# Optimization experiments

Hardware: AMD Instinct MI355X
Metric: run time of the kernel (lower is better)

Reference implementation:

```python
import jax, jax.numpy as jnp
import numpy as np

B, T = 64, 512
V, D, H = 50000, 256, 256  # vocab, word-embed dim, LSTM hidden


def _lstm_dir(x, Wih, Whh, bih, bhh):
    """Unidirectional LSTM over time (PyTorch gate order i,f,g,o). x: [B,T,D_in] -> [B,T,H]."""
    xp = jnp.einsum('btd,gd->btg', x, Wih) + bih + bhh  # precompute input projections [B,T,4H]
    xp = xp.transpose(1, 0, 2)  # [T,B,4H]
    Hh = Whh.shape[1]
    h0 = jnp.zeros((x.shape[0], Hh), x.dtype)

    def step(carry, xt):
        h, c = carry
        g = xt + h @ Whh.T
        i, f, gg, o = jnp.split(g, 4, axis=-1)
        c = jax.nn.sigmoid(f) * c + jax.nn.sigmoid(i) * jnp.tanh(gg)
        h = jax.nn.sigmoid(o) * jnp.tanh(c)
        return (h, c), h

    _, hs = jax.lax.scan(step, (h0, h0), xp)
    return hs.transpose(1, 0, 2)  # [B,T,H]


def _bidir(x, rev_idx, pf, pb):
    """Length-aware bidirectional layer: reverse only the valid prefix (emulates pack_padded_sequence)."""
    hf = _lstm_dir(x, *pf)
    xr = jnp.take_along_axis(x, rev_idx[..., None], axis=1)   # reversed valid prefix
    hb = _lstm_dir(xr, *pb)
    hb = jnp.take_along_axis(hb, rev_idx[..., None], axis=1)  # flip back (involution on valid part)
    return jnp.concatenate([hf, hb], axis=-1)  # [B,T,2H]


def setup_inputs() -> dict:
    key = jax.random.key(0)
    ks = jax.random.split(key, 24)
    x = jax.random.randint(ks[0], (B, T), 0, V - 1)          # avoid padding_idx = V-1
    sentlen = jax.random.randint(ks[1], (B,), 1, T + 1)       # ragged lengths in [1, T]
    embed = (jax.random.normal(ks[2], (V, D), jnp.float32) * 0.1).at[V - 1].set(0.0)
    inp = {"x": x, "sentlen": sentlen, "embed": embed}
    k = 3
    for layer, in_dim in [(0, D), (1, 2 * H)]:
        for d in ["f", "b"]:
            s = 1.0 / np.sqrt(H)
            inp[f"Wih{layer}{d}"] = jax.random.uniform(ks[k], (4 * H, in_dim), jnp.float32, -s, s); k += 1
            inp[f"Whh{layer}{d}"] = jax.random.uniform(ks[k], (4 * H, H), jnp.float32, -s, s); k += 1
            inp[f"bih{layer}{d}"] = jax.random.uniform(ks[k], (4 * H,), jnp.float32, -s, s); k += 1
            inp[f"bhh{layer}{d}"] = jax.random.uniform(ks[k], (4 * H,), jnp.float32, -s, s); k += 1
    return inp


def reference(x, sentlen, embed,
              Wih0f, Whh0f, bih0f, bhh0f, Wih0b, Whh0b, bih0b, bhh0b,
              Wih1f, Whh1f, bih1f, bhh1f, Wih1b, Whh1b, bih1b, bhh1b):
    emb = embed[x]  # [B,T,D]; dropout is a no-op in eval mode
    t = jnp.arange(x.shape[1])
    valid = t[None, :] < sentlen[:, None]                       # [B,T]
    rev_idx = jnp.where(valid, sentlen[:, None] - 1 - t[None, :], t[None, :])
    h1 = _bidir(emb, rev_idx, (Wih0f, Whh0f, bih0f, bhh0f), (Wih0b, Whh0b, bih0b, bhh0b))
    h2 = _bidir(h1, rev_idx, (Wih1f, Whh1f, bih1f, bhh1f), (Wih1b, Whh1b, bih1b, bhh1b))
    # ragged max-pool over valid positions (replaces the per-sample Python loop)
    feat = jnp.max(jnp.where(valid[..., None], h2, -jnp.inf), axis=1)  # [B,2H]
    return feat[None]  # [1,B,2H]
```

## Files before the change

kernel.cpp:

```cpp
#include <hip/hip_runtime.h>
#include <stdint.h>
#include <stddef.h>

#define BATCH 64
#define TT    512
#define DIM   256
#define HID   256
#define MROWS (BATCH*TT)

typedef unsigned short u16;
typedef unsigned int u32;
typedef __attribute__((ext_vector_type(8))) short  short8;
typedef __attribute__((ext_vector_type(4))) float  f32x4;
typedef __attribute__((ext_vector_type(4))) int    int4v;
typedef __attribute__((ext_vector_type(4))) unsigned short u16x4;

__device__ __forceinline__ u16 bf16_hi(float f) {
    union { float f; unsigned u; } v; v.f = f;
    unsigned r = v.u + 0x7fffu + ((v.u >> 16) & 1u);
    return (u16)(r >> 16);
}
__device__ __forceinline__ float bf16f(u16 b) {
    union { unsigned u; float f; } v; v.u = ((unsigned)b) << 16;
    return v.f;
}
__device__ __forceinline__ float fsigmoid(float x) { return 1.f / (1.f + __expf(-x)); }
__device__ __forceinline__ float ftanh(float x) {
    x = fminf(15.f, fmaxf(-15.f, x));
    float e = __expf(2.f * x);
    return (e - 1.f) / (e + 1.f);
}

__global__ __launch_bounds__(256) void k_prep(
    const float* __restrict__ Wih0f, const float* __restrict__ Whh0f, const float* __restrict__ bih0f, const float* __restrict__ bhh0f,
    const float* __restrict__ Wih0b, const float* __restrict__ Whh0b, const float* __restrict__ bih0b, const float* __restrict__ bhh0b,
    const float* __restrict__ Wih1f, const float* __restrict__ Whh1f, const float* __restrict__ bih1f, const float* __restrict__ bhh1f,
    const float* __restrict__ Wih1b, const float* __restrict__ Whh1b, const float* __restrict__ bih1b, const float* __restrict__ bhh1b,
    u16* __restrict__ WihQ0hi, u16* __restrict__ WihQ0lo,
    u16* __restrict__ WhhQ0hi, u16* __restrict__ WhhQ0lo,
    u16* __restrict__ WihQ1hi, u16* __restrict__ WihQ1lo,
    u16* __restrict__ WhhQ1hi, u16* __restrict__ WhhQ1lo,
    float* __restrict__ bsum, u32* __restrict__ hxp)
{
    const int i = blockIdx.x * 256 + threadIdx.x;
    if (i < 2621440) {
        const float* srcf; const float* srcb; u16* dhi; u16* dlo; int off; int K;
        if      (i <  524288) { srcf = Wih0f; srcb = Wih0b; dhi = WihQ0hi; dlo = WihQ0lo; off = i;           K = 256; }
        else if (i < 1048576) { srcf = Whh0f; srcb = Whh0b; dhi = WhhQ0hi; dlo = WhhQ0lo; off = i -  524288; K = 256; }
        else if (i < 2097152) { srcf = Wih1f; srcb = Wih1b; dhi = WihQ1hi; dlo = WihQ1lo; off = i - 1048576; K = 512; }
        else                  { srcf = Whh1f; srcb = Whh1b; dhi = WhhQ1hi; dlo = WhhQ1lo; off = i - 2097152; K = 256; }
        const int SZ = 1024 * K;
        const int dd = off / SZ;
        const int o  = off - dd * SZ;
        const int pr = o / K;
        const int k  = o - pr * K;
        const int s  = pr >> 6;
        const int ww = (pr >> 4) & 3;
        const int m  = pr & 15;
        const int src_row = (m & 3) * 256 + s * 16 + ww * 4 + (m >> 2);
        const float v = (dd ? srcb : srcf)[src_row * K + k];
        const u16 h = bf16_hi(v);
        dhi[off] = h;
        dlo[off] = bf16_hi(v - bf16f(h));
    } else if (i < 2621440 + 4096) {
        const int j = i - 2621440;
        const float* bihs[4] = { bih0f, bih0b, bih1f, bih1b };
        const float* bhhs[4] = { bhh0f, bhh0b, bhh1f, bhh1b };
        const int ld = j >> 10, k = j & 1023;
        bsum[j] = bihs[ld][k] + bhhs[ld][k];
    } else if (i < 2621440 + 4096 + 131072) {
        const int j = i - (2621440 + 4096);
        hxp[j] = ((j >> 15) & 1) ? 0x00010000u : 0u;
    }
}

__global__ __launch_bounds__(256) void k_gather(
    const int* __restrict__ x, const float* __restrict__ embed, u16* __restrict__ A0)
{
    const int row = blockIdx.x * 4 + (threadIdx.x >> 6);
    const int col = (threadIdx.x & 63) * 4;
    const int xi = x[row];
    const f32x4 v = *(const f32x4*)(embed + (size_t)xi * DIM + col);
    u16x4 h;
    #pragma unroll
    for (int i = 0; i < 4; i++) h[i] = bf16_hi(v[i]);
    *(u16x4*)(A0 + (size_t)row * DIM + col) = h;
}

template<int KIN, bool WRITE_H, bool POOL>
__global__ __launch_bounds__(256, 1) void k_lstm(
    const u16* __restrict__ Xin,
    const u16* __restrict__ WhhHi, const u16* __restrict__ WhhLo,
    const u16* __restrict__ WihHi, const u16* __restrict__ WihLo,
    const float* __restrict__ bsum,
    const int* __restrict__ slen,
    u16* __restrict__ H0,
    float* __restrict__ outp,
    u32* __restrict__ hx)
{
    constexpr int KV = KIN / 32;
    constexpr int CR = KIN / 8;
    constexpr int NST = (16 * CR) / 256;

    const int bid = blockIdx.x;
    const int s = bid >> 3;
    const int d = (bid >> 2) & 1;
    const int c = bid & 3;
    const int tid = threadIdx.x;
    const int l = tid & 63, w = tid >> 6;

    __shared__ u16 xs[16 * KIN];
    __shared__ u16 hs_hi[16 * 256];
    __shared__ u16 hs_lo[16 * 256];
    __shared__ u32 ho_pack[16 * 17];
    __shared__ int lens_sh[16];
    __shared__ int maxlen_sh;

    if (tid < 16) lens_sh[tid] = slen[c * 16 + tid];
    __syncthreads();
    if (tid == 0) {
        int m = 0;
        #pragma unroll
        for (int i = 0; i < 16; i++) m = max(m, lens_sh[i]);
        maxlen_sh = m;
    }
    __syncthreads();
    const int maxlen = maxlen_sh;

    const int wblk = (d * 16 + s) * 4 + w;
    short8 wfh[8], wfl[8];
    #pragma unroll
    for (int kv = 0; kv < 8; kv++) {
        const size_t off = (size_t)(wblk * 16 + (l & 15)) * 256 + kv * 32 + ((l >> 4) << 3);
        wfh[kv] = *(const short8*)(WhhHi + off);
        wfl[kv] = *(const short8*)(WhhLo + off);
    }
    short8 uih[KV], uil[KV];
    #pragma unroll
    for (int kv = 0; kv < KV; kv++) {
        const size_t off = (size_t)(wblk * 16 + (l & 15)) * KIN + kv * 32 + ((l >> 4) << 3);
        uih[kv] = *(const short8*)(WihHi + off);
        uil[kv] = *(const short8*)(WihLo + off);
    }
    #pragma unroll
    for (int kv = 0; kv < 8; kv++) asm volatile("" : "+v"(wfh[kv]), "+v"(wfl[kv]));
    #pragma unroll
    for (int kv = 0; kv < KV; kv++) asm volatile("" : "+v"(uih[kv]), "+v"(uil[kv]));

    const int q_u  = l >> 4;
    const int bi_m = l & 15;
    const int unit = s * 16 + w * 4 + q_u;
    float bias_g[4];
    #pragma unroll
    for (int g = 0; g < 4; g++) bias_g[g] = bsum[d * 1024 + g * 256 + unit];

    float creg = 0.f, mx = -1e30f;
    const int swz = bi_m & 7;
    const int klane = l >> 4;
    const int len_m = lens_sh[bi_m];

    for (int t = 0; t < maxlen; ++t) {
        short8 xreg[NST];
        #pragma unroll
        for (int p = 0; p < NST; p++) {
            const int idx = p * 256 + tid;
            const int bi = idx / CR;
            const int ch = idx - bi * CR;
            const int len_b = lens_sh[bi];
            const int pos = (d == 0) ? t : ((t < len_b) ? (len_b - 1 - t) : t);
            xreg[p] = *(const short8*)(Xin + ((size_t)(c * 16 + bi) * TT + pos) * KIN + ch * 8);
            asm volatile("" : "+v"(xreg[p]));
        }

        if (t == 0) {
            const short8 z = {0,0,0,0,0,0,0,0};
            for (int i = tid; i < 512; i += 256) {
                ((short8*)hs_hi)[i] = z;
                ((short8*)hs_lo)[i] = z;
            }
        } else {
            const u32* gbase = hx + (((size_t)(t & 1) * 2 + d) * 64 + c * 16) * 256;
            const u32* p0 = gbase + tid * 4;
            const u32* p1 = p0 + 1024;
            const u32* p2 = p0 + 2048;
            const u32* p3 = p0 + 3072;
            const int expect = (t >> 1) & 1;
            int4v w0, w1, w2, w3;
            int rounds = 0;
            for (;;) {
                asm volatile(
                    "global_load_dwordx4 %0, %4, off sc0 sc1\n\t"
                    "global_load_dwordx4 %1, %5, off sc0 sc1\n\t"
                    "global_load_dwordx4 %2, %6, off sc0 sc1\n\t"
                    "global_load_dwordx4 %3, %7, off sc0 sc1"
                    : "=&v"(w0), "=&v"(w1), "=&v"(w2), "=&v"(w3)
                    : "v"(p0), "v"(p1), "v"(p2), "v"(p3)
                    : "memory");
                asm volatile("s_waitcnt vmcnt(0)"
                    : "+v"(w0), "+v"(w1), "+v"(w2), "+v"(w3) :: "memory");
                u32 aw = 0xFFFFFFFFu, ow = 0u;
                #pragma unroll
                for (int j = 0; j < 4; j++) {
                    aw &= (u32)w0[j]; ow |= (u32)w0[j];
                    aw &= (u32)w1[j]; ow |= (u32)w1[j];
                    aw &= (u32)w2[j]; ow |= (u32)w2[j];
                    aw &= (u32)w3[j]; ow |= (u32)w3[j];
                }
                const int ok = expect ? (int)((aw >> 16) & 1u)
                                      : (int)(((ow >> 16) & 1u) ^ 1u);
                if (__all(ok)) break;
                if (++rounds > (1 << 17)) break;
                __builtin_amdgcn_s_sleep(1);
            }
            const int u0 = (tid & 63) * 4;
            const int ch = u0 >> 3;
            const int co = u0 & 7;
            int4v wq[4] = {w0, w1, w2, w3};
            #pragma unroll
            for (int qq = 0; qq < 4; qq++) {
                const int bi = qq * 4 + (tid >> 6);
                u16x4 hi4, lo4;
                #pragma unroll
                for (int j = 0; j < 4; j++) {
                    const u32 wd = (u32)wq[qq][j];
                    hi4[j] = (u16)(wd & 0xFFFFu);
                    lo4[j] = (u16)(wd >> 16);
                }
                *(u16x4*)(hs_hi + bi * 256 + (ch ^ (bi & 7)) * 8 + co) = hi4;
                *(u16x4*)(hs_lo + bi * 256 + (ch ^ (bi & 7)) * 8 + co) = lo4;
            }
        }
        #pragma unroll
        for (int p = 0; p < NST; p++) {
            const int idx = p * 256 + tid;
            const int bi = idx / CR;
            const int ch = idx - bi * CR;
            *(short8*)(xs + bi * KIN + (ch ^ (bi & 7)) * 8) = xreg[p];
        }
        __syncthreads();

        f32x4 acc_a = {0.f,0.f,0.f,0.f}, acc_b = {0.f,0.f,0.f,0.f}, acc_c = {0.f,0.f,0.f,0.f};
        #pragma unroll
        for (int kv = 0; kv < 8; kv++) {
            const int kc = kv * 4 + klane;
            const short8 bh = *(const short8*)(hs_hi + bi_m * 256 + (kc ^ swz) * 8);
            const short8 bl = *(const short8*)(hs_lo + bi_m * 256 + (kc ^ swz) * 8);
            acc_a = __builtin_amdgcn_mfma_f32_16x16x32_bf16(wfh[kv], bh, acc_a, 0, 0, 0);
            acc_b = __builtin_amdgcn_mfma_f32_16x16x32_bf16(wfl[kv], bh, acc_b, 0, 0, 0);
            acc_c = __builtin_amdgcn_mfma_f32_16x16x32_bf16(wfh[kv], bl, acc_c, 0, 0, 0);
        }
        #pragma unroll
        for (int kv = 0; kv < KV; kv++) {
            const int kc = kv * 4 + klane;
            const short8 bx = *(const short8*)(xs + bi_m * KIN + (kc ^ swz) * 8);
            acc_a = __builtin_amdgcn_mfma_f32_16x16x32_bf16(uih[kv], bx, acc_a, 0, 0, 0);
            acc_b = __builtin_amdgcn_mfma_f32_16x16x32_bf16(uil[kv], bx, acc_b, 0, 0, 0);
        }

        {
            const float gi = acc_a[0] + acc_b[0] + acc_c[0] + bias_g[0];
            const float gf = acc_a[1] + acc_b[1] + acc_c[1] + bias_g[1];
            const float gg = acc_a[2] + acc_b[2] + acc_c[2] + bias_g[2];
            const float go = acc_a[3] + acc_b[3] + acc_c[3] + bias_g[3];
            const float cc = fsigmoid(gf) * creg + fsigmoid(gi) * ftanh(gg);
            creg = cc;
            const float h = fsigmoid(go) * ftanh(cc);
            if (POOL && t < len_m) mx = fmaxf(mx, h);
            const u16 hh = bf16_hi(h);
            const u32 hl = ((u32)bf16_hi(h - bf16f(hh)) & 0xFFFEu) | (u32)(((t + 1) >> 1) & 1);
            ho_pack[bi_m * 17 + w * 4 + q_u] = (u32)hh | (hl << 16);
        }
        __syncthreads();

        if (w == 0) {
            const int bi = l >> 2, qq = l & 3;
            const int4v pv = *(const int4v*)(ho_pack + bi * 17 + qq * 4);
            u32* dst = hx + (((size_t)((t + 1) & 1) * 2 + d) * 64 + c * 16 + bi) * 256 + s * 16 + qq * 4;
            asm volatile("global_store_dwordx4 %0, %1, off sc0 sc1" :: "v"(dst), "v"(pv) : "memory");
        } else if (WRITE_H && w == 1) {
            const int bi = l >> 2, qq = l & 3;
            const int4v pv = *(const int4v*)(ho_pack + bi * 17 + qq * 4);
            u16x4 hv;
            #pragma unroll
            for (int j = 0; j < 4; j++) hv[j] = (u16)((u32)pv[j] & 0xFFFFu);
            const int len_b = lens_sh[bi];
            const int pos = (d == 0) ? t : ((t < len_b) ? (len_b - 1 - t) : t);
            *(u16x4*)(H0 + ((size_t)(c * 16 + bi) * TT + pos) * 512 + d * 256 + s * 16 + qq * 4) = hv;
        }
    }

    if (POOL) {
        outp[(size_t)(c * 16 + bi_m) * 512 + d * 256 + unit] = mx;
    }
}

extern "C" void kernel_launch(void* const* d_in, const int* in_sizes, int n_in,
                              void* d_out, int out_size, void* d_ws, size_t ws_size,
                              hipStream_t stream)
{
    (void)in_sizes; (void)n_in; (void)out_size; (void)ws_size;
    const int*   x     = (const int*)d_in[0];
    const int*   slen  = (const int*)d_in[1];
    const float* embed = (const float*)d_in[2];
    const float* W[16];
    for (int i = 0; i < 16; i++) W[i] = (const float*)d_in[3 + i];
    float* out = (float*)d_out;

    char* p = (char*)d_ws;
    u16* A0      = (u16*)p;   p += (size_t)MROWS * DIM * 2;
    u16* H0      = (u16*)p;   p += (size_t)MROWS * 512 * 2;
    u16* WihQ0hi = (u16*)p;   p += 524288 * 2;
    u16* WihQ0lo = (u16*)p;   p += 524288 * 2;
    u16* WhhQ0hi = (u16*)p;   p += 524288 * 2;
    u16* WhhQ0lo = (u16*)p;   p += 524288 * 2;
    u16* WihQ1hi = (u16*)p;   p += 1048576 * 2;
    u16* WihQ1lo = (u16*)p;   p += 1048576 * 2;
    u16* WhhQ1hi = (u16*)p;   p += 524288 * 2;
    u16* WhhQ1lo = (u16*)p;   p += 524288 * 2;
    float* bsum  = (float*)p; p += 4096 * 4;
    u32* hxp     = (u32*)p;   p += 131072 * 4;

    k_prep<<<10768, 256, 0, stream>>>(
        W[0], W[1], W[2], W[3], W[4], W[5], W[6], W[7],
        W[8], W[9], W[10], W[11], W[12], W[13], W[14], W[15],
        WihQ0hi, WihQ0lo, WhhQ0hi, WhhQ0lo, WihQ1hi, WihQ1lo, WhhQ1hi, WhhQ1lo,
        bsum, hxp);

    k_gather<<<8192, 256, 0, stream>>>(x, embed, A0);

    k_lstm<256, true, false><<<128, 256, 0, stream>>>(
        A0, WhhQ0hi, WhhQ0lo, WihQ0hi, WihQ0lo, bsum, slen,
        H0, nullptr, hxp);

    k_lstm<512, false, true><<<128, 256, 0, stream>>>(
        H0, WhhQ1hi, WhhQ1lo, WihQ1hi, WihQ1lo, bsum + 2048, slen,
        nullptr, out, hxp + 65536);
}
```

Before: 2.673 ms.

## Assign LSTM work groups to blocks by XCD and poll hidden state via local cache

Launches 256 blocks instead of 128. Each block reads its XCC id from a hardware register and claims a slot through atomic counters, so each group of 16 cooperating blocks (one direction and batch chunk) lands on the same XCD; surplus blocks wait for all arrivals, fill any unfilled slots, or exit. The per-step hidden-state exchange then polls with non-coherent 'nt' loads that can hit the shared XCD-local L2, and writers also issue a plain store alongside the system-coherent one. After 512 failed polls a block falls back to the old coherent loads with sleep. This aims to cut cross-XCD coherence latency in the per-timestep handshake, but depends on undocumented XCC_ID register behaviour, adds a startup spin barrier, and risks stale reads or extra stalls if the placement assumption does not hold.

```diff
diff --git a/kernel.cpp b/kernel.cpp
--- a/kernel.cpp
+++ b/kernel.cpp
@@ -7,6 +7,7 @@
 #define DIM   256
 #define HID   256
 #define MROWS (BATCH*TT)
+#define NBLK  256
 
 typedef unsigned short u16;
 typedef unsigned int u32;
@@ -40,7 +41,7 @@
     u16* __restrict__ WhhQ0hi, u16* __restrict__ WhhQ0lo,
     u16* __restrict__ WihQ1hi, u16* __restrict__ WihQ1lo,
     u16* __restrict__ WhhQ1hi, u16* __restrict__ WhhQ1lo,
-    float* __restrict__ bsum, u32* __restrict__ hxp)
+    float* __restrict__ bsum, u32* __restrict__ hxp, u32* __restrict__ ctlp)
 {
     const int i = blockIdx.x * 256 + threadIdx.x;
     if (i < 2621440) {
@@ -71,6 +72,9 @@
     } else if (i < 2621440 + 4096 + 131072) {
         const int j = i - (2621440 + 4096);
         hxp[j] = ((j >> 15) & 1) ? 0x00010000u : 0u;
+    } else if (i < 2621440 + 4096 + 131072 + 1024) {
+        const int j = i - (2621440 + 4096 + 131072);
+        ctlp[j] = ((j & 511) < 16) ? 0u : 0xFFFFFFFFu;
     }
 }
 
@@ -96,16 +100,13 @@
     const int* __restrict__ slen,
     u16* __restrict__ H0,
     float* __restrict__ outp,
-    u32* __restrict__ hx)
+    u32* __restrict__ hx,
+    u32* __restrict__ ctl)
 {
     constexpr int KV = KIN / 32;
     constexpr int CR = KIN / 8;
     constexpr int NST = (16 * CR) / 256;
 
-    const int bid = blockIdx.x;
-    const int s = bid >> 3;
-    const int d = (bid >> 2) & 1;
-    const int c = bid & 3;
     const int tid = threadIdx.x;
     const int l = tid & 63, w = tid >> 6;
 
@@ -115,6 +116,38 @@
     __shared__ u32 ho_pack[16 * 17];
     __shared__ int lens_sh[16];
     __shared__ int maxlen_sh;
+    __shared__ int asg[3];
+
+    if (tid == 0) {
+        u32 xcc;
+        asm volatile("s_getreg_b32 %0, hwreg(20, 0, 32)" : "=s"(xcc));
+        xcc &= 7u;
+        const u32 r = __hip_atomic_fetch_add(&ctl[xcc], 1u, __ATOMIC_RELAXED, __HIP_MEMORY_SCOPE_AGENT);
+        __hip_atomic_fetch_add(&ctl[8], 1u, __ATOMIC_RELAXED, __HIP_MEMORY_SCOPE_AGENT);
+        int g = 0, s = 0, run = 0;
+        if (r < 16u) { g = (int)xcc; s = (int)r; run = 1; }
+        else {
+            const u32 r2 = __hip_atomic_fetch_add(&ctl[9], 1u, __ATOMIC_RELAXED, __HIP_MEMORY_SCOPE_AGENT);
+            int spins = 0;
+            while (__hip_atomic_load(&ctl[8], __ATOMIC_RELAXED, __HIP_MEMORY_SCOPE_AGENT) < (u32)NBLK) {
+                __builtin_amdgcn_s_sleep(2);
+                if (++spins > (1 << 20)) break;
+            }
+            u32 idx = r2;
+            for (int x2 = 0; x2 < 8; x2++) {
+                const u32 cl = __hip_atomic_load(&ctl[x2], __ATOMIC_RELAXED, __HIP_MEMORY_SCOPE_AGENT);
+                const u32 have = cl > 16u ? 16u : cl;
+                const u32 def = 16u - have;
+                if (idx < def) { g = x2; s = (int)(have + idx); run = 1; break; }
+                idx -= def;
+            }
+        }
+        asg[0] = run; asg[1] = g; asg[2] = s;
+    }
+    __syncthreads();
+    if (!asg[0]) return;
+    const int g = asg[1], s = asg[2];
+    const int d = g >> 2, c = g & 3;
 
     if (tid < 16) lens_sh[tid] = slen[c * 16 + tid];
     __syncthreads();
@@ -152,12 +185,13 @@
     const int unit = s * 16 + w * 4 + q_u;
     float bias_g[4];
     #pragma unroll
-    for (int g = 0; g < 4; g++) bias_g[g] = bsum[d * 1024 + g * 256 + unit];
+    for (int gg2 = 0; gg2 < 4; gg2++) bias_g[gg2] = bsum[d * 1024 + gg2 * 256 + unit];
 
     float creg = 0.f, mx = -1e30f;
     const int swz = bi_m & 7;
     const int klane = l >> 4;
     const int len_m = lens_sh[bi_m];
+    int fastmode = 1;
 
     for (int t = 0; t < maxlen; ++t) {
         short8 xreg[NST];
@@ -188,14 +222,25 @@
             int4v w0, w1, w2, w3;
             int rounds = 0;
             for (;;) {
-                asm volatile(
-                    "global_load_dwordx4 %0, %4, off sc0 sc1\n\t"
-                    "global_load_dwordx4 %1, %5, off sc0 sc1\n\t"
-                    "global_load_dwordx4 %2, %6, off sc0 sc1\n\t"
-                    "global_load_dwordx4 %3, %7, off sc0 sc1"
-                    : "=&v"(w0), "=&v"(w1), "=&v"(w2), "=&v"(w3)
-                    : "v"(p0), "v"(p1), "v"(p2), "v"(p3)
-                    : "memory");
+                if (fastmode) {
+                    asm volatile(
+                        "global_load_dwordx4 %0, %4, off nt\n\t"
+                        "global_load_dwordx4 %1, %5, off nt\n\t"
+                        "global_load_dwordx4 %2, %6, off nt\n\t"
+                        "global_load_dwordx4 %3, %7, off nt"
+                        : "=&v"(w0), "=&v"(w1), "=&v"(w2), "=&v"(w3)
+                        : "v"(p0), "v"(p1), "v"(p2), "v"(p3)
+                        : "memory");
+                } else {
+                    asm volatile(
+                        "global_load_dwordx4 %0, %4, off sc0 sc1\n\t"
+                        "global_load_dwordx4 %1, %5, off sc0 sc1\n\t"
+                        "global_load_dwordx4 %2, %6, off sc0 sc1\n\t"
+                        "global_load_dwordx4 %3, %7, off sc0 sc1"
+                        : "=&v"(w0), "=&v"(w1), "=&v"(w2), "=&v"(w3)
+                        : "v"(p0), "v"(p1), "v"(p2), "v"(p3)
+                        : "memory");
+                }
                 asm volatile("s_waitcnt vmcnt(0)"
                     : "+v"(w0), "+v"(w1), "+v"(w2), "+v"(w3) :: "memory");
                 u32 aw = 0xFFFFFFFFu, ow = 0u;
@@ -209,8 +254,13 @@
                 const int ok = expect ? (int)((aw >> 16) & 1u)
                                       : (int)(((ow >> 16) & 1u) ^ 1u);
                 if (__all(ok)) break;
-                if (++rounds > (1 << 17)) break;
-                __builtin_amdgcn_s_sleep(1);
+                ++rounds;
+                if (fastmode) {
+                    if (rounds > 512) { fastmode = 0; rounds = 0; }
+                } else {
+                    if (rounds > 8192) break;
+                    __builtin_amdgcn_s_sleep(1);
+                }
             }
             const int u0 = (tid & 63) * 4;
             const int ch = u0 >> 3;
@@ -277,6 +327,7 @@
             const int4v pv = *(const int4v*)(ho_pack + bi * 17 + qq * 4);
             u32* dst = hx + (((size_t)((t + 1) & 1) * 2 + d) * 64 + c * 16 + bi) * 256 + s * 16 + qq * 4;
             asm volatile("global_store_dwordx4 %0, %1, off sc0 sc1" :: "v"(dst), "v"(pv) : "memory");
+            asm volatile("global_store_dwordx4 %0, %1, off" :: "v"(dst), "v"(pv) : "memory");
         } else if (WRITE_H && w == 1) {
             const int bi = l >> 2, qq = l & 3;
             const int4v pv = *(const int4v*)(ho_pack + bi * 17 + qq * 4);
@@ -319,20 +370,21 @@
     u16* WhhQ1lo = (u16*)p;   p += 524288 * 2;
     float* bsum  = (float*)p; p += 4096 * 4;
     u32* hxp     = (u32*)p;   p += 131072 * 4;
-
-    k_prep<<<10768, 256, 0, stream>>>(
+    u32* ctlp    = (u32*)p;   p += 1024 * 4;
+
+    k_prep<<<10772, 256, 0, stream>>>(
         W[0], W[1], W[2], W[3], W[4], W[5], W[6], W[7],
         W[8], W[9], W[10], W[11], W[12], W[13], W[14], W[15],
         WihQ0hi, WihQ0lo, WhhQ0hi, WhhQ0lo, WihQ1hi, WihQ1lo, WhhQ1hi, WhhQ1lo,
-        bsum, hxp);
+        bsum, hxp, ctlp);
 
     k_gather<<<8192, 256, 0, stream>>>(x, embed, A0);
 
-    k_lstm<256, true, false><<<128, 256, 0, stream>>>(
+    k_lstm<256, true, false><<<NBLK, 256, 0, stream>>>(
         A0, WhhQ0hi, WhhQ0lo, WihQ0hi, WihQ0lo, bsum, slen,
-        H0, nullptr, hxp);
-
-    k_lstm<512, false, true><<<128, 256, 0, stream>>>(
+        H0, nullptr, hxp, ctlp);
+
+    k_lstm<512, false, true><<<NBLK, 256, 0, stream>>>(
         H0, WhhQ1hi, WhhQ1lo, WihQ1hi, WihQ1lo, bsum + 2048, slen,
-        nullptr, out, hxp + 65536);
-}
+        nullptr, out, hxp + 65536, ctlp + 512);
+}
```

Result: slower. 3.071 ms (+14.9%).

## Compute input-projection MFMAs before the cross-block wait and prefetch next x

Applied to the files above, without the earlier changes.

The input-projection contribution for step t is now computed at the top of the iteration, from an x tile staged in LDS during the previous step, before waiting for the other blocks' hidden state. The x rows for step t+1 are loaded while the hidden-state exchange is in flight, so x-load latency and the U·x MFMAs overlap with the inter-block synchronization. A cheap single-dword flag spin by 16 lanes runs before the full hidden-state load, and the sleep in the main spin now happens only every 64 rounds. The cost is an extra __syncthreads per step and tighter retry limits, which could break out of the spin before the data is ready.

```diff
diff --git a/kernel.cpp b/kernel.cpp
--- a/kernel.cpp
+++ b/kernel.cpp
@@ -152,14 +152,35 @@
     const int unit = s * 16 + w * 4 + q_u;
     float bias_g[4];
     #pragma unroll
-    for (int g = 0; g < 4; g++) bias_g[g] = bsum[d * 1024 + g * 256 + unit];
+    for (int gg2 = 0; gg2 < 4; gg2++) bias_g[gg2] = bsum[d * 1024 + gg2 * 256 + unit];
 
     float creg = 0.f, mx = -1e30f;
     const int swz = bi_m & 7;
     const int klane = l >> 4;
     const int len_m = lens_sh[bi_m];
 
+    #pragma unroll
+    for (int p = 0; p < NST; p++) {
+        const int idx = p * 256 + tid;
+        const int bi = idx / CR;
+        const int ch = idx - bi * CR;
+        const int len_b = lens_sh[bi];
+        const int pos = (d == 0) ? 0 : (len_b - 1);
+        const short8 v = *(const short8*)(Xin + ((size_t)(c * 16 + bi) * TT + pos) * KIN + ch * 8);
+        *(short8*)(xs + bi * KIN + (ch ^ (bi & 7)) * 8) = v;
+    }
+    __syncthreads();
+
     for (int t = 0; t < maxlen; ++t) {
+        f32x4 acc_a = {0.f,0.f,0.f,0.f}, acc_b = {0.f,0.f,0.f,0.f}, acc_c = {0.f,0.f,0.f,0.f};
+        #pragma unroll
+        for (int kv = 0; kv < KV; kv++) {
+            const int kc = kv * 4 + klane;
+            const short8 bx = *(const short8*)(xs + bi_m * KIN + (kc ^ swz) * 8);
+            acc_a = __builtin_amdgcn_mfma_f32_16x16x32_bf16(uih[kv], bx, acc_a, 0, 0, 0);
+            acc_b = __builtin_amdgcn_mfma_f32_16x16x32_bf16(uil[kv], bx, acc_b, 0, 0, 0);
+        }
+
         short8 xreg[NST];
         #pragma unroll
         for (int p = 0; p < NST; p++) {
@@ -167,7 +188,8 @@
             const int bi = idx / CR;
             const int ch = idx - bi * CR;
             const int len_b = lens_sh[bi];
-            const int pos = (d == 0) ? t : ((t < len_b) ? (len_b - 1 - t) : t);
+            int pos = (d == 0) ? (t + 1) : (((t + 1) < len_b) ? (len_b - 1 - (t + 1)) : (t + 1));
+            if (pos > TT - 1) pos = TT - 1;
             xreg[p] = *(const short8*)(Xin + ((size_t)(c * 16 + bi) * TT + pos) * KIN + ch * 8);
             asm volatile("" : "+v"(xreg[p]));
         }
@@ -180,11 +202,27 @@
             }
         } else {
             const u32* gbase = hx + (((size_t)(t & 1) * 2 + d) * 64 + c * 16) * 256;
+            const int expect = (t >> 1) & 1;
+            {
+                const u32* sp = gbase + (l & 15) * 16;
+                int cr2 = 0;
+                for (;;) {
+                    int ok = 1;
+                    if (l < 16) {
+                        u32 v;
+                        asm volatile("global_load_dword %0, %1, off sc0 sc1"
+                                     : "=v"(v) : "v"(sp) : "memory");
+                        asm volatile("s_waitcnt vmcnt(0)" : "+v"(v) :: "memory");
+                        ok = ((int)((v >> 16) & 1u) == expect);
+                    }
+                    if (__all(ok)) break;
+                    if (++cr2 > 4096) break;
+                }
+            }
             const u32* p0 = gbase + tid * 4;
             const u32* p1 = p0 + 1024;
             const u32* p2 = p0 + 2048;
             const u32* p3 = p0 + 3072;
-            const int expect = (t >> 1) & 1;
             int4v w0, w1, w2, w3;
             int rounds = 0;
             for (;;) {
@@ -209,8 +247,9 @@
                 const int ok = expect ? (int)((aw >> 16) & 1u)
                                       : (int)(((ow >> 16) & 1u) ^ 1u);
                 if (__all(ok)) break;
-                if (++rounds > (1 << 17)) break;
-                __builtin_amdgcn_s_sleep(1);
+                ++rounds;
+                if (rounds > 8192) break;
+                if ((rounds & 63) == 63) __builtin_amdgcn_s_sleep(1);
             }
             const int u0 = (tid & 63) * 4;
             const int ch = u0 >> 3;
@@ -230,16 +269,8 @@
                 *(u16x4*)(hs_lo + bi * 256 + (ch ^ (bi & 7)) * 8 + co) = lo4;
             }
         }
-        #pragma unroll
-        for (int p = 0; p < NST; p++) {
-            const int idx = p * 256 + tid;
-            const int bi = idx / CR;
-            const int ch = idx - bi * CR;
-            *(short8*)(xs + bi * KIN + (ch ^ (bi & 7)) * 8) = xreg[p];
-        }
         __syncthreads();
 
-        f32x4 acc_a = {0.f,0.f,0.f,0.f}, acc_b = {0.f,0.f,0.f,0.f}, acc_c = {0.f,0.f,0.f,0.f};
         #pragma unroll
         for (int kv = 0; kv < 8; kv++) {
             const int kc = kv * 4 + klane;
@@ -248,13 +279,6 @@
             acc_a = __builtin_amdgcn_mfma_f32_16x16x32_bf16(wfh[kv], bh, acc_a, 0, 0, 0);
             acc_b = __builtin_amdgcn_mfma_f32_16x16x32_bf16(wfl[kv], bh, acc_b, 0, 0, 0);
             acc_c = __builtin_amdgcn_mfma_f32_16x16x32_bf16(wfh[kv], bl, acc_c, 0, 0, 0);
-        }
-        #pragma unroll
-        for (int kv = 0; kv < KV; kv++) {
-            const int kc = kv * 4 + klane;
-            const short8 bx = *(const short8*)(xs + bi_m * KIN + (kc ^ swz) * 8);
-            acc_a = __builtin_amdgcn_mfma_f32_16x16x32_bf16(uih[kv], bx, acc_a, 0, 0, 0);
-            acc_b = __builtin_amdgcn_mfma_f32_16x16x32_bf16(uil[kv], bx, acc_b, 0, 0, 0);
         }
 
         {
@@ -287,6 +311,15 @@
             const int pos = (d == 0) ? t : ((t < len_b) ? (len_b - 1 - t) : t);
             *(u16x4*)(H0 + ((size_t)(c * 16 + bi) * TT + pos) * 512 + d * 256 + s * 16 + qq * 4) = hv;
         }
+
+        #pragma unroll
+        for (int p = 0; p < NST; p++) {
+            const int idx = p * 256 + tid;
+            const int bi = idx / CR;
+            const int ch = idx - bi * CR;
+            *(short8*)(xs + bi * KIN + (ch ^ (bi & 7)) * 8) = xreg[p];
+        }
+        __syncthreads();
     }
 
     if (POOL) {
```

Result: slower. 2.840 ms (+6.2%).
